# Performance work log

Measured on AMD Instinct MI355X. Metric: run time of the kernel, lower is better.

The kernel has to match this reference:

```python
import jax, jax.numpy as jnp
import numpy as np

N_QUBITS = 8


def setup_inputs() -> dict:
    key = jax.random.key(0)
    k1, k2, k3, k4 = jax.random.split(key, 4)
    B, S, E, F = 4, 4096, 1024, 4096
    x = jax.random.normal(k1, (B, S, E), dtype=jnp.float32)
    theta = jax.random.normal(k2, (N_QUBITS,), dtype=jnp.float32)
    # nn.Linear default init scale ~ 1/sqrt(fan_in)
    w1 = jax.random.normal(k3, (F, N_QUBITS), dtype=jnp.float32) / np.sqrt(N_QUBITS)
    w2 = jax.random.normal(k4, (E, F), dtype=jnp.float32) / np.sqrt(F)
    return {"x": x, "theta": theta, "w1": w1, "w2": w2}


def reference(x, theta, w1, w2):
    # Quantum circuit per wire i: |0> -RX(x_i)-> -RY(theta_i)-> <Z>
    # No entangling gates, so <Z_i> = cos(x_i) * cos(theta_i) exactly.
    q_vecs = jnp.cos(x[..., :N_QUBITS]) * jnp.cos(theta)  # [B,S,nq]
    h = jax.nn.relu(jnp.einsum('bsq,fq->bsf', q_vecs, w1))  # [B,S,F]
    # dropout is identity in eval mode
    out = jnp.einsum('bsf,ef->bse', h, w2)  # [B,S,E]
    return out
```

## Files before the change

kernel.cpp:

```cpp
#include <hip/hip_runtime.h>
#include <hip/hip_bf16.h>


#define M_TOTAL 16384
#define E_DIM 1024
#define F_DIM 4096
#define NQ 8

typedef __attribute__((ext_vector_type(8))) short bf16x8;
typedef __attribute__((ext_vector_type(8))) unsigned short ushort8;
typedef __attribute__((ext_vector_type(4))) float f32x4;

__device__ __forceinline__ unsigned short f2bf(float f) {
  union { float f; unsigned u; } c; c.f = f;
  unsigned u = c.u + (0x7fffu + ((c.u >> 16) & 1u));
  return (unsigned short)(u >> 16);
}

__global__ __launch_bounds__(256) void w2cvt_kernel(
    const float* __restrict__ w2, unsigned short* __restrict__ w2bf) {
  size_t i = ((size_t)blockIdx.x * 256 + threadIdx.x) * 8;
  float v[8];
  *(float4*)&v[0] = *(const float4*)&w2[i];
  *(float4*)&v[4] = *(const float4*)&w2[i + 4];
  ushort8 p;
#pragma unroll
  for (int j = 0; j < 8; ++j) p[j] = f2bf(v[j]);
  *(ushort8*)&w2bf[i] = p;
}

__global__ __launch_bounds__(256) void qrelu_kernel(
    const float* __restrict__ x, const float* __restrict__ theta,
    const float* __restrict__ w1, unsigned short* __restrict__ A, int m_base) {
  __shared__ float qv[32][NQ];
  const int t = threadIdx.x;
  const int m0 = m_base + blockIdx.x * 32;
  {
    const int ml = t >> 3, q = t & 7;
    float xv = x[(size_t)(m0 + ml) * 1024 + q];
    qv[ml][q] = cosf(xv) * cosf(theta[q]);
  }
  __syncthreads();

  for (int oi = 0; oi < 2; ++oi) {
    const int o = t + oi * 256;
    float w[64];
#pragma unroll
    for (int i = 0; i < 16; ++i)
      *(float4*)&w[i * 4] = *(const float4*)&w1[o * 64 + i * 4];
    for (int ml = 0; ml < 32; ++ml) {
      ushort8 pk;
#pragma unroll
      for (int j = 0; j < 8; ++j) {
        float s = 0.f;
#pragma unroll
        for (int q = 0; q < NQ; ++q) s = fmaf(qv[ml][q], w[j * 8 + q], s);
        pk[j] = f2bf(s > 0.f ? s : 0.f);
      }
      *(ushort8*)&A[(size_t)(m0 - m_base + ml) * F_DIM + o * 8] = pk;
    }
  }
}

#define BAR __builtin_amdgcn_s_barrier()
#define VM0 asm volatile("s_waitcnt vmcnt(0)" ::: "memory")

#define GLDS(src, dst) \
  __builtin_amdgcn_global_load_lds( \
      (const __attribute__((address_space(1))) void*)(src), \
      (__attribute__((address_space(3))) void*)(dst), 16, 0, 0)

#define STAGE_ALL(buf) do { \
  GLDS(pA0, &As[buf][0][wid * 512]); \
  GLDS(pA1, &As[buf][0][4096 + wid * 512]); \
  GLDS(pA2, &As[buf][1][wid * 512]); \
  GLDS(pA3, &As[buf][1][4096 + wid * 512]); \
  GLDS(pB0, &Bs[buf][0][wid * 512]); \
  GLDS(pB1, &Bs[buf][0][4096 + wid * 512]); \
  GLDS(pB2, &Bs[buf][1][wid * 512]); \
  GLDS(pB3, &Bs[buf][1][4096 + wid * 512]); \
  pA0 += 64; pA1 += 64; pA2 += 64; pA3 += 64; \
  pB0 += 64; pB1 += 64; pB2 += 64; pB3 += 64; \
} while (0)

#define RDA(buf, mt, kk) \
  (*(const bf16x8*)&asW[(buf) * 16384 + (mt) * 1024 + ((kk) ? aO1 : aO0)])
#define RDB(buf, nt, kk) \
  (*(const bf16x8*)&bsW[(buf) * 16384 + (nt) * 1024 + ((kk) ? bO1 : bO0)])

#define STEP(buf, kk, mt) do { \
  if ((mt) < 6) af3[((mt) + 2) % 3] = RDA(buf, (mt) + 2, kk); \
  __builtin_amdgcn_s_setprio(1); \
  acc[mt][0] = __builtin_amdgcn_mfma_f32_16x16x32_bf16( \
      af3[(mt) % 3], bf4[0], acc[mt][0], 0, 0, 0); \
  acc[mt][1] = __builtin_amdgcn_mfma_f32_16x16x32_bf16( \
      af3[(mt) % 3], bf4[1], acc[mt][1], 0, 0, 0); \
  acc[mt][2] = __builtin_amdgcn_mfma_f32_16x16x32_bf16( \
      af3[(mt) % 3], bf4[2], acc[mt][2], 0, 0, 0); \
  acc[mt][3] = __builtin_amdgcn_mfma_f32_16x16x32_bf16( \
      af3[(mt) % 3], bf4[3], acc[mt][3], 0, 0, 0); \
  __builtin_amdgcn_s_setprio(0); \
  __builtin_amdgcn_sched_barrier(0); \
} while (0)

#define HALF(buf, kk) do { \
  bf16x8 af3[3], bf4[4]; \
  bf4[0] = RDB(buf, 0, kk); \
  bf4[1] = RDB(buf, 1, kk); \
  bf4[2] = RDB(buf, 2, kk); \
  bf4[3] = RDB(buf, 3, kk); \
  af3[0] = RDA(buf, 0, kk); \
  af3[1] = RDA(buf, 1, kk); \
  STEP(buf, kk, 0); STEP(buf, kk, 1); STEP(buf, kk, 2); STEP(buf, kk, 3); \
  STEP(buf, kk, 4); STEP(buf, kk, 5); STEP(buf, kk, 6); STEP(buf, kk, 7); \
} while (0)

#define REGION(buf) do { \
  HALF(buf, 0); \
  HALF(buf, 1); \
  VM0; \
  BAR; \
} while (0)

__global__ __launch_bounds__(512, 2) void gemm_kernel(
    const unsigned short* __restrict__ Abf, const unsigned short* __restrict__ w2bf,
    float* __restrict__ out, int m_base) {
  __shared__ __align__(16) unsigned short As[2][2][128 * 64];
  __shared__ __align__(16) unsigned short Bs[2][2][128 * 64];

  const int tid = threadIdx.x;
  const int lane = tid & 63;
  const int wid = tid >> 6;
  const int wr = wid >> 2;
  const int wc = wid & 3;

  const int nwg = gridDim.x;
  const int bid = blockIdx.x;
  const int qq = nwg >> 3, rr = nwg & 7;
  const int xcd = bid & 7, sub = bid >> 3;
  const int wgid =
      (xcd < rr ? xcd * (qq + 1) : rr * (qq + 1) + (xcd - rr) * qq) + sub;
  const int mb = wgid >> 2;
  const int nb = wgid & 3;

  const unsigned short* Ag = Abf + (size_t)mb * 256 * F_DIM;
  const unsigned short* Bg = w2bf + (size_t)nb * 256 * F_DIM;

  f32x4 acc[8][4] = {};

  const int hi4 = lane >> 4, l7 = lane & 7, l15 = lane & 15;
  const int aO0 = l15 * 64 + ((hi4 ^ l7) << 3);
  const int aO1 = aO0 ^ 32;
  const int bO0 = ((wc & 1) * 64 + l15) * 64 + ((hi4 ^ l7) << 3);
  const int bO1 = bO0 ^ 32;
  const unsigned short* asW = &As[0][wr][0];
  const unsigned short* bsW = &Bs[0][wc >> 1][0];

  const int srow = tid >> 3;
  const int sc = (tid & 7) ^ (srow & 7);
  const unsigned short* pA0 = Ag + (size_t)(srow)*F_DIM + sc * 8;
  const unsigned short* pA1 = Ag + (size_t)(64 + srow) * F_DIM + sc * 8;
  const unsigned short* pA2 = Ag + (size_t)(128 + srow) * F_DIM + sc * 8;
  const unsigned short* pA3 = Ag + (size_t)(192 + srow) * F_DIM + sc * 8;
  const unsigned short* pB0 = Bg + (size_t)(srow)*F_DIM + sc * 8;
  const unsigned short* pB1 = Bg + (size_t)(64 + srow) * F_DIM + sc * 8;
  const unsigned short* pB2 = Bg + (size_t)(128 + srow) * F_DIM + sc * 8;
  const unsigned short* pB3 = Bg + (size_t)(192 + srow) * F_DIM + sc * 8;

  STAGE_ALL(0);
  VM0;
  BAR;

#pragma unroll 1
  for (int t2 = 0; t2 < 32; ++t2) {
    STAGE_ALL(1);
    REGION(0);
    if (t2 < 31) STAGE_ALL(0);
    REGION(1);
  }

  const int cl = lane & 15, rg = lane >> 4;
  float* ob = out + (size_t)(m_base + mb * 256 + wr * 128) * E_DIM + nb * 256 +
              wc * 64 + cl;
#pragma unroll
  for (int mt = 0; mt < 8; ++mt)
#pragma unroll
    for (int r = 0; r < 4; ++r) {
      float* orow = ob + (size_t)(mt * 16 + rg * 4 + r) * E_DIM;
#pragma unroll
      for (int nt = 0; nt < 4; ++nt) orow[nt * 16] = acc[mt][nt][r];
    }
}

extern "C" void kernel_launch(void* const* d_in, const int* in_sizes, int n_in,
                              void* d_out, int out_size, void* d_ws, size_t ws_size,
                              hipStream_t stream) {
  const float* x = (const float*)d_in[0];
  const float* theta = (const float*)d_in[1];
  const float* w1 = (const float*)d_in[2];
  const float* w2 = (const float*)d_in[3];
  float* out = (float*)d_out;

  unsigned short* w2bf = (unsigned short*)d_ws;
  unsigned short* A = w2bf + (size_t)E_DIM * F_DIM;

  size_t abytes = ws_size - (size_t)E_DIM * F_DIM * 2;
  size_t maxrows = abytes / ((size_t)F_DIM * 2);
  int Mc = (int)((maxrows / 256) * 256);
  if (Mc > M_TOTAL) Mc = M_TOTAL;
  if (Mc < 256) Mc = 256;

  w2cvt_kernel<<<E_DIM * F_DIM / 2048, 256, 0, stream>>>(w2, w2bf);

  for (int mb = 0; mb < M_TOTAL; mb += Mc) {
    int rows = M_TOTAL - mb < Mc ? M_TOTAL - mb : Mc;
    qrelu_kernel<<<rows / 32, 256, 0, stream>>>(x, theta, w1, A, mb);
    gemm_kernel<<<(rows / 256) * 4, 512, 0, stream>>>(A, w2bf, out, mb);
  }
}
```

Before: 156.3 us.

## Load B operand directly from global into registers, stage only A in LDS

Removes the LDS staging buffers for the w2 (B) operand. Each wave now reads its B fragments straight from global memory into registers, and only A tiles go through global_load_lds double buffering. The block-to-tile mapping is also changed so consecutive workgroups share the same N block, which should keep the B panel hot in L2. This halves LDS traffic and footprint, but puts global-load latency on the MFMA critical path, and B reads are no longer shared across the two waves that use the same columns.

```diff
diff --git a/kernel.cpp b/kernel.cpp
--- a/kernel.cpp
+++ b/kernel.cpp
@@ -63,6 +63,7 @@
 }
 
 #define BAR __builtin_amdgcn_s_barrier()
+#define SB __builtin_amdgcn_sched_barrier(0)
 #define VM0 asm volatile("s_waitcnt vmcnt(0)" ::: "memory")
 
 #define GLDS(src, dst) \
@@ -70,54 +71,50 @@
       (const __attribute__((address_space(1))) void*)(src), \
       (__attribute__((address_space(3))) void*)(dst), 16, 0, 0)
 
-#define STAGE_ALL(buf) do { \
+#define STAGE_A(buf) do { \
   GLDS(pA0, &As[buf][0][wid * 512]); \
   GLDS(pA1, &As[buf][0][4096 + wid * 512]); \
   GLDS(pA2, &As[buf][1][wid * 512]); \
   GLDS(pA3, &As[buf][1][4096 + wid * 512]); \
-  GLDS(pB0, &Bs[buf][0][wid * 512]); \
-  GLDS(pB1, &Bs[buf][0][4096 + wid * 512]); \
-  GLDS(pB2, &Bs[buf][1][wid * 512]); \
-  GLDS(pB3, &Bs[buf][1][4096 + wid * 512]); \
   pA0 += 64; pA1 += 64; pA2 += 64; pA3 += 64; \
-  pB0 += 64; pB1 += 64; pB2 += 64; pB3 += 64; \
+  SB; \
 } while (0)
 
 #define RDA(buf, mt, kk) \
   (*(const bf16x8*)&asW[(buf) * 16384 + (mt) * 1024 + ((kk) ? aO1 : aO0)])
-#define RDB(buf, nt, kk) \
-  (*(const bf16x8*)&bsW[(buf) * 16384 + (nt) * 1024 + ((kk) ? bO1 : bO0)])
 
 #define STEP(buf, kk, mt) do { \
   if ((mt) < 6) af3[((mt) + 2) % 3] = RDA(buf, (mt) + 2, kk); \
   __builtin_amdgcn_s_setprio(1); \
   acc[mt][0] = __builtin_amdgcn_mfma_f32_16x16x32_bf16( \
-      af3[(mt) % 3], bf4[0], acc[mt][0], 0, 0, 0); \
+      af3[(mt) % 3], bq[0], acc[mt][0], 0, 0, 0); \
   acc[mt][1] = __builtin_amdgcn_mfma_f32_16x16x32_bf16( \
-      af3[(mt) % 3], bf4[1], acc[mt][1], 0, 0, 0); \
+      af3[(mt) % 3], bq[1], acc[mt][1], 0, 0, 0); \
   acc[mt][2] = __builtin_amdgcn_mfma_f32_16x16x32_bf16( \
-      af3[(mt) % 3], bf4[2], acc[mt][2], 0, 0, 0); \
+      af3[(mt) % 3], bq[2], acc[mt][2], 0, 0, 0); \
   acc[mt][3] = __builtin_amdgcn_mfma_f32_16x16x32_bf16( \
-      af3[(mt) % 3], bf4[3], acc[mt][3], 0, 0, 0); \
+      af3[(mt) % 3], bq[3], acc[mt][3], 0, 0, 0); \
   __builtin_amdgcn_s_setprio(0); \
-  __builtin_amdgcn_sched_barrier(0); \
-} while (0)
-
-#define HALF(buf, kk) do { \
-  bf16x8 af3[3], bf4[4]; \
-  bf4[0] = RDB(buf, 0, kk); \
-  bf4[1] = RDB(buf, 1, kk); \
-  bf4[2] = RDB(buf, 2, kk); \
-  bf4[3] = RDB(buf, 3, kk); \
+  SB; \
+} while (0)
+
+#define HALF(buf, kk, OFS) do { \
+  bf16x8 bq[4], af3[3]; \
+  bq[0] = *(const bf16x8*)(pB0_ + (OFS)); \
+  bq[1] = *(const bf16x8*)(pB1_ + (OFS)); \
+  bq[2] = *(const bf16x8*)(pB2_ + (OFS)); \
+  bq[3] = *(const bf16x8*)(pB3_ + (OFS)); \
   af3[0] = RDA(buf, 0, kk); \
   af3[1] = RDA(buf, 1, kk); \
   STEP(buf, kk, 0); STEP(buf, kk, 1); STEP(buf, kk, 2); STEP(buf, kk, 3); \
   STEP(buf, kk, 4); STEP(buf, kk, 5); STEP(buf, kk, 6); STEP(buf, kk, 7); \
 } while (0)
 
-#define REGION(buf) do { \
-  HALF(buf, 0); \
-  HALF(buf, 1); \
+#define REGION(buf, PREF) do { \
+  if (PREF) STAGE_A((buf) ^ 1); \
+  HALF(buf, 0, 0); \
+  HALF(buf, 1, 32); \
+  pB0_ += 64; pB1_ += 64; pB2_ += 64; pB3_ += 64; \
   VM0; \
   BAR; \
 } while (0)
@@ -126,7 +123,6 @@
     const unsigned short* __restrict__ Abf, const unsigned short* __restrict__ w2bf,
     float* __restrict__ out, int m_base) {
   __shared__ __align__(16) unsigned short As[2][2][128 * 64];
-  __shared__ __align__(16) unsigned short Bs[2][2][128 * 64];
 
   const int tid = threadIdx.x;
   const int lane = tid & 63;
@@ -140,21 +136,18 @@
   const int xcd = bid & 7, sub = bid >> 3;
   const int wgid =
       (xcd < rr ? xcd * (qq + 1) : rr * (qq + 1) + (xcd - rr) * qq) + sub;
-  const int mb = wgid >> 2;
-  const int nb = wgid & 3;
+  const int mbmax = nwg >> 2;
+  const int nbk = wgid / mbmax;
+  const int mb = wgid % mbmax;
 
   const unsigned short* Ag = Abf + (size_t)mb * 256 * F_DIM;
-  const unsigned short* Bg = w2bf + (size_t)nb * 256 * F_DIM;
 
   f32x4 acc[8][4] = {};
 
   const int hi4 = lane >> 4, l7 = lane & 7, l15 = lane & 15;
   const int aO0 = l15 * 64 + ((hi4 ^ l7) << 3);
   const int aO1 = aO0 ^ 32;
-  const int bO0 = ((wc & 1) * 64 + l15) * 64 + ((hi4 ^ l7) << 3);
-  const int bO1 = bO0 ^ 32;
   const unsigned short* asW = &As[0][wr][0];
-  const unsigned short* bsW = &Bs[0][wc >> 1][0];
 
   const int srow = tid >> 3;
   const int sc = (tid & 7) ^ (srow & 7);
@@ -162,25 +155,27 @@
   const unsigned short* pA1 = Ag + (size_t)(64 + srow) * F_DIM + sc * 8;
   const unsigned short* pA2 = Ag + (size_t)(128 + srow) * F_DIM + sc * 8;
   const unsigned short* pA3 = Ag + (size_t)(192 + srow) * F_DIM + sc * 8;
-  const unsigned short* pB0 = Bg + (size_t)(srow)*F_DIM + sc * 8;
-  const unsigned short* pB1 = Bg + (size_t)(64 + srow) * F_DIM + sc * 8;
-  const unsigned short* pB2 = Bg + (size_t)(128 + srow) * F_DIM + sc * 8;
-  const unsigned short* pB3 = Bg + (size_t)(192 + srow) * F_DIM + sc * 8;
-
-  STAGE_ALL(0);
+
+  const size_t bRow = (size_t)(nbk * 256 + wc * 64 + l15);
+  const unsigned short* pB0_ = w2bf + (bRow + 0) * F_DIM + hi4 * 8;
+  const unsigned short* pB1_ = w2bf + (bRow + 16) * F_DIM + hi4 * 8;
+  const unsigned short* pB2_ = w2bf + (bRow + 32) * F_DIM + hi4 * 8;
+  const unsigned short* pB3_ = w2bf + (bRow + 48) * F_DIM + hi4 * 8;
+
+  STAGE_A(0);
   VM0;
   BAR;
 
 #pragma unroll 1
-  for (int t2 = 0; t2 < 32; ++t2) {
-    STAGE_ALL(1);
-    REGION(0);
-    if (t2 < 31) STAGE_ALL(0);
-    REGION(1);
-  }
+  for (int t2 = 0; t2 < 31; ++t2) {
+    REGION(0, 1);
+    REGION(1, 1);
+  }
+  REGION(0, 1);
+  REGION(1, 0);
 
   const int cl = lane & 15, rg = lane >> 4;
-  float* ob = out + (size_t)(m_base + mb * 256 + wr * 128) * E_DIM + nb * 256 +
+  float* ob = out + (size_t)(m_base + mb * 256 + wr * 128) * E_DIM + nbk * 256 +
               wc * 64 + cl;
 #pragma unroll
   for (int mt = 0; mt < 8; ++mt)
```

Result: slower. 215.6 us (+38.0%).
